# Kernel optimization log

Measured on AMD Instinct MI355X. Metric: run time of the kernel, lower is better.

Reference implementation:

```python
import jax, jax.numpy as jnp
import numpy as np

N_NODES = 50000
N_EDGES = 800000
DIM = 96
N_LAYERS = 3
N_GRAPHS = 128
OUT_DIM = 10


def setup_inputs() -> dict:
    key = jax.random.key(0)
    ks = jax.random.split(key, 9)
    s = 1.0 / np.sqrt(DIM)
    return {
        "x": jax.random.normal(ks[0], (N_NODES, DIM), dtype=jnp.float32),
        "edge_index": jax.random.randint(ks[1], (2, N_EDGES), 0, N_NODES, dtype=jnp.int32),
        "batch": jnp.sort(jax.random.randint(ks[2], (N_NODES,), 0, N_GRAPHS, dtype=jnp.int32)),
        "W1": jax.random.normal(ks[3], (N_LAYERS, DIM, DIM), dtype=jnp.float32) * s,
        "W2": jax.random.normal(ks[4], (N_LAYERS, DIM, DIM), dtype=jnp.float32) * s,
        "cw1": jax.random.normal(ks[5], (DIM, DIM), dtype=jnp.float32) * s,
        "cb1": jax.random.normal(ks[6], (DIM,), dtype=jnp.float32) * s,
        "cw2": jax.random.normal(ks[7], (DIM, OUT_DIM), dtype=jnp.float32) * s,
        "cb2": jax.random.normal(ks[8], (OUT_DIM,), dtype=jnp.float32) * s,
    }


def reference(x, edge_index, batch, W1, W2, cw1, cb1, cw2, cb2):
    src, dst = edge_index[0], edge_index[1]
    h = x
    for l in range(N_LAYERS):
        self_part = h @ W1[l]                       # [N, D]
        # transform at node level then gather per edge (same math as per-edge W2(x_j))
        msg = (h @ W2[l])[src]                      # [E, D]
        neighbor_part = jax.ops.segment_sum(msg, dst, num_segments=N_NODES)
        h = jax.nn.relu(self_part + neighbor_part)
    graph_emb = jax.ops.segment_sum(h, batch, num_segments=N_GRAPHS)  # [G, D]
    hidden = jax.nn.relu(graph_emb @ cw1 + cb1)
    return hidden @ cw2 + cb2                       # [G, OUT_DIM]
```

## Files before the change

### kernel.cpp

```cpp
#include <hip/hip_runtime.h>

#define N_NODES   50000
#define N_EDGES   800000
#define DIM       96
#define N_GRAPHS  128
#define OUT_DIM   10
#define NPAD      50048
#define NBINS     391
#define P1_BLOCKS 128
#define EPB       (N_EDGES / P1_BLOCKS)
#define SLICECAP  48
#define CAP       64
#define LPAD      104

#define CAST_NB   ((N_NODES * 12 + 255) / 256)
#define CONV_NB   ((3 * DIM * 2 * DIM + 255) / 256)

typedef __attribute__((ext_vector_type(8))) short          short8;
typedef __attribute__((ext_vector_type(8))) unsigned short u16x8;
typedef __attribute__((ext_vector_type(4))) float          f32x4;

__device__ __forceinline__ float b2f(unsigned short u) {
    union { unsigned int i; float f; } v; v.i = ((unsigned int)u) << 16; return v.f;
}
__device__ __forceinline__ unsigned short f2b(float f) {
    union { float f; unsigned int i; } v; v.f = f;
    unsigned int u = v.i;
    return (unsigned short)((u + 0x7fffu + ((u >> 16) & 1u)) >> 16);
}

__global__ __launch_bounds__(256) void prep(const float* __restrict__ x,
                                            const float* __restrict__ W1,
                                            const float* __restrict__ W2,
                                            unsigned short* __restrict__ harr,
                                            unsigned short* __restrict__ Bt)
{
    const int b = blockIdx.x;
    const int t = threadIdx.x;
    if (b < CAST_NB) {
        const int tid = b * 256 + t;
        if (tid >= N_NODES * 12) return;
        const int node = tid / 12;
        const int c    = (tid - node * 12) * 8;
        const float4 v0 = *(const float4*)(x + (size_t)node * DIM + c);
        const float4 v1 = *(const float4*)(x + (size_t)node * DIM + c + 4);
        u16x8 o;
        o[0] = f2b(v0.x); o[1] = f2b(v0.y); o[2] = f2b(v0.z); o[3] = f2b(v0.w);
        o[4] = f2b(v1.x); o[5] = f2b(v1.y); o[6] = f2b(v1.z); o[7] = f2b(v1.w);
        *(u16x8*)(harr + (size_t)node * DIM + c) = o;
    } else {
        const int idx = (b - CAST_NB) * 256 + t;
        if (idx >= 3 * DIM * 2 * DIM) return;
        const int l   = idx / (DIM * 2 * DIM);
        const int rem = idx - l * (DIM * 2 * DIM);
        const int n   = rem / (2 * DIM);
        const int k   = rem - n * (2 * DIM);
        const float v = (k < DIM) ? W1[(size_t)l * DIM * DIM + k * DIM + n]
                                  : W2[(size_t)l * DIM * DIM + (k - DIM) * DIM + n];
        Bt[idx] = f2b(v);
    }
}

__global__ __launch_bounds__(256) void pass1_bin(const int* __restrict__ src,
                                                 const int* __restrict__ dst,
                                                 int* __restrict__ binned,
                                                 int* __restrict__ cnt)
{
    __shared__ int cur[NBINS];
    const int t   = threadIdx.x;
    const int blk = blockIdx.x;
    const int e0  = blk * EPB;

    for (int b = t; b < NBINS; b += 256) cur[b] = 0;
    __syncthreads();

    for (int e = e0 + t; e < e0 + EPB; e += 256) {
        const int d   = dst[e];
        const int bin = d >> 7;
        const int pos = atomicAdd(&cur[bin], 1);
        if (pos < SLICECAP)
            binned[((size_t)bin * P1_BLOCKS + blk) * SLICECAP + pos]
                = ((d & 127) << 16) | src[e];
    }
    __syncthreads();

    for (int b = t; b < NBINS; b += 256)
        cnt[b * P1_BLOCKS + blk] = min(cur[b], SLICECAP);
}

__global__ __launch_bounds__(256) void pass2_scatter(const int* __restrict__ cnt,
                                                     const int* __restrict__ binned,
                                                     int* __restrict__ csrc,
                                                     int* __restrict__ deg)
{
    __shared__ int buf[2][P1_BLOCKS];
    __shared__ int soff[P1_BLOCKS + 1];
    __shared__ int ncnt[128];
    const int bin = blockIdx.x;
    const int t   = threadIdx.x;
    const int n0  = bin << 7;

    if (t < P1_BLOCKS) { buf[0][t] = cnt[bin * P1_BLOCKS + t]; ncnt[t] = 0; }
    __syncthreads();

    int c = 0;
#pragma unroll
    for (int off = 1; off < P1_BLOCKS; off <<= 1) {
        if (t < P1_BLOCKS) {
            int x = buf[c][t];
            if (t >= off) x += buf[c][t - off];
            buf[c ^ 1][t] = x;
        }
        __syncthreads();
        c ^= 1;
    }
    if (t < P1_BLOCKS) { soff[t + 1] = buf[c][t]; if (t == 0) soff[0] = 0; }
    __syncthreads();

    const int Eb = soff[P1_BLOCKS];
    for (int i = t; i < Eb; i += 256) {
        int lo = 0, hi = P1_BLOCKS - 1;
        while (lo < hi) { int mid = (lo + hi + 1) >> 1;
                          if (soff[mid] <= i) lo = mid; else hi = mid - 1; }
        const int v    = binned[((size_t)bin * P1_BLOCKS + lo) * SLICECAP + (i - soff[lo])];
        const int dlow = v >> 16;
        const int s    = v & 0xffff;
        const int pos  = atomicAdd(&ncnt[dlow], 1);
        if (pos < CAP) csrc[(size_t)(n0 + dlow) * CAP + pos] = s;
    }
    __syncthreads();

    if (t < 128 && n0 + t < N_NODES) deg[n0 + t] = min(ncnt[t], CAP);
}

__global__ __launch_bounds__(384) void gnn_layer(
    const unsigned short* __restrict__ harr, const int* __restrict__ deg,
    const int* __restrict__ csrc, const unsigned short* __restrict__ Btl,
    unsigned short* __restrict__ hout)
{
    __shared__ unsigned short aggLds[64][LPAD];
    const int t       = threadIdx.x;
    const int rowBase = blockIdx.x * 64;

    const int lane = t & 63;
    const int w    = t >> 6;
    const int m    = lane & 15;
    const int q    = lane >> 4;
    short8 bfrag[6];
#pragma unroll
    for (int s = 0; s < 6; s++)
        bfrag[s] = *(const short8*)(Btl + (size_t)(w * 16 + m) * (2 * DIM) + s * 32 + q * 8);

    {
        const int r    = t / 6;
        const int sub  = t - r * 6;
        const int node = rowBase + r;
        const int off  = sub * 16;

        float a[16];
#pragma unroll
        for (int i = 0; i < 16; i++) a[i] = 0.f;

        if (node < N_NODES) {
            const int d = deg[node];
            const int* __restrict__ bkt = csrc + (size_t)node * CAP;
            const unsigned short* __restrict__ hb = harr + off;

            const int nfull = d & ~3;
            int c = 0;
            for (; c < nfull; c += 4) {
                const int4 s = *(const int4*)(bkt + c);
                const unsigned short* p0 = hb + (size_t)s.x * DIM;
                const unsigned short* p1 = hb + (size_t)s.y * DIM;
                const unsigned short* p2 = hb + (size_t)s.z * DIM;
                const unsigned short* p3 = hb + (size_t)s.w * DIM;
                const u16x8 va0 = *(const u16x8*)(p0), vb0 = *(const u16x8*)(p0 + 8);
                const u16x8 va1 = *(const u16x8*)(p1), vb1 = *(const u16x8*)(p1 + 8);
                const u16x8 va2 = *(const u16x8*)(p2), vb2 = *(const u16x8*)(p2 + 8);
                const u16x8 va3 = *(const u16x8*)(p3), vb3 = *(const u16x8*)(p3 + 8);
#pragma unroll
                for (int i = 0; i < 8; i++) {
                    a[i]     += b2f(va0[i]) + b2f(va1[i]) + b2f(va2[i]) + b2f(va3[i]);
                    a[i + 8] += b2f(vb0[i]) + b2f(vb1[i]) + b2f(vb2[i]) + b2f(vb3[i]);
                }
            }
            for (; c < d; c++) {
                const unsigned short* p0 = hb + (size_t)bkt[c] * DIM;
                const u16x8 va0 = *(const u16x8*)(p0), vb0 = *(const u16x8*)(p0 + 8);
#pragma unroll
                for (int i = 0; i < 8; i++) {
                    a[i]     += b2f(va0[i]);
                    a[i + 8] += b2f(vb0[i]);
                }
            }
        }

        u16x8 o0, o1;
#pragma unroll
        for (int i = 0; i < 8; i++) { o0[i] = f2b(a[i]); o1[i] = f2b(a[i + 8]); }
        *(u16x8*)(&aggLds[r][off])     = o0;
        *(u16x8*)(&aggLds[r][off + 8]) = o1;
    }
    __syncthreads();

#pragma unroll
    for (int r = 0; r < 4; r++) {
        const int rb = rowBase + r * 16;
        f32x4 acc = {0.f, 0.f, 0.f, 0.f};
        const unsigned short* ah = harr + (size_t)(rb + m) * DIM + q * 8;
#pragma unroll
        for (int s = 0; s < 3; s++) {
            const short8 af = *(const short8*)(ah + s * 32);
            acc = __builtin_amdgcn_mfma_f32_16x16x32_bf16(af, bfrag[s], acc, 0, 0, 0);
        }
#pragma unroll
        for (int s = 0; s < 3; s++) {
            const short8 af = *(const short8*)(&aggLds[r * 16 + m][s * 32 + q * 8]);
            acc = __builtin_amdgcn_mfma_f32_16x16x32_bf16(af, bfrag[s + 3], acc, 0, 0, 0);
        }
#pragma unroll
        for (int i = 0; i < 4; i++) {
            const int grow = rb + q * 4 + i;
            if (grow < N_NODES)
                hout[(size_t)grow * DIM + w * 16 + m] = f2b(fmaxf(acc[i], 0.f));
        }
    }
}

__global__ __launch_bounds__(384) void pool_classify(
    const unsigned short* __restrict__ h, const int* __restrict__ batch,
    const float* __restrict__ cw1, const float* __restrict__ cb1,
    const float* __restrict__ cw2, const float* __restrict__ cb2,
    float* __restrict__ out)
{
    const int g = blockIdx.x;
    const int t = threadIdx.x;

    int lo = 0, hi = N_NODES;
    while (lo < hi) { int m = (lo + hi) >> 1; if (batch[m] < g) lo = m + 1; else hi = m; }
    const int start = lo;
    hi = N_NODES;
    while (lo < hi) { int m = (lo + hi) >> 1; if (batch[m] < g + 1) lo = m + 1; else hi = m; }
    const int end = lo;

    __shared__ float part[4][DIM];
    __shared__ float gr[DIM];
    __shared__ float hid[DIM];

    const int col = t % DIM;
    const int ty  = t / DIM;

    float s = 0.f;
    for (int n = start + ty; n < end; n += 4)
        s += b2f(h[(size_t)n * DIM + col]);
    part[ty][col] = s;
    __syncthreads();
    if (ty == 0)
        gr[col] = part[0][col] + part[1][col] + part[2][col] + part[3][col];
    __syncthreads();

    float hsum = 0.f;
    const int k0 = ty * (DIM / 4);
#pragma unroll 4
    for (int k = k0; k < k0 + DIM / 4; k++)
        hsum += gr[k] * cw1[k * DIM + col];
    part[ty][col] = hsum;
    __syncthreads();
    if (ty == 0)
        hid[col] = fmaxf(part[0][col] + part[1][col] + part[2][col] + part[3][col]
                         + cb1[col], 0.f);
    __syncthreads();

    if (t < OUT_DIM) {
        float o = cb2[t];
#pragma unroll 4
        for (int k = 0; k < DIM; k++) o += hid[k] * cw2[k * OUT_DIM + t];
        out[g * OUT_DIM + t] = o;
    }
}

extern "C" void kernel_launch(void* const* d_in, const int* in_sizes, int n_in,
                              void* d_out, int out_size, void* d_ws, size_t ws_size,
                              hipStream_t stream)
{
    const float* x     = (const float*)d_in[0];
    const int*   ei    = (const int*)  d_in[1];
    const int*   batch = (const int*)  d_in[2];
    const float* W1    = (const float*)d_in[3];
    const float* W2    = (const float*)d_in[4];
    const float* cw1   = (const float*)d_in[5];
    const float* cb1   = (const float*)d_in[6];
    const float* cw2   = (const float*)d_in[7];
    const float* cb2   = (const float*)d_in[8];
    float*       out   = (float*)d_out;

    const int* src = ei;
    const int* dst = ei + N_EDGES;

    unsigned short* bufA = (unsigned short*)d_ws;
    unsigned short* bufB = bufA + (size_t)NPAD * DIM;
    unsigned short* Bt   = bufB + (size_t)NPAD * DIM;
    int*   cnt    = (int*)(Bt + 3 * DIM * 2 * DIM);
    int*   binned = cnt + NBINS * P1_BLOCKS;
    int*   csrc   = binned + (size_t)NBINS * P1_BLOCKS * SLICECAP;
    int*   deg    = csrc + (size_t)N_NODES * CAP;

    prep<<<CAST_NB + CONV_NB, 256, 0, stream>>>(x, W1, W2, bufA, Bt);
    pass1_bin<<<P1_BLOCKS, 256, 0, stream>>>(src, dst, binned, cnt);
    pass2_scatter<<<NBINS, 256, 0, stream>>>(cnt, binned, csrc, deg);

    unsigned short* hin  = bufA;
    unsigned short* hout = bufB;
    for (int l = 0; l < 3; l++) {
        gnn_layer<<<NPAD / 64, 384, 0, stream>>>(hin, deg, csrc,
                                                 Bt + (size_t)l * DIM * 2 * DIM, hout);
        unsigned short* tmp = hin; hin = hout; hout = tmp;
    }

    pool_classify<<<N_GRAPHS, 384, 0, stream>>>(hin, batch, cw1, cb1, cw2, cb2, out);
}
```

Before: 275.9 us.

## Fuse prep with edge binning, simplify scatter, coalesce layer stores, widen pooling

The edge-binning pass is merged into the prep kernel so the x cast, weight transpose and binning share one launch. Pass2 drops its prefix scan and binary search and instead gives each slice to two threads that read it directly. The layer kernel stages its ReLU output in LDS and writes rows with 16-byte vector stores instead of scattered 2-byte stores. Pooling runs 960 threads per graph to spread the node reduction wider. The costs are an extra LDS round trip with two barriers per layer block, and pass2 load imbalance across slices.

```diff
diff --git a/kernel.cpp b/kernel.cpp
--- a/kernel.cpp
+++ b/kernel.cpp
@@ -29,16 +29,34 @@
     return (unsigned short)((u + 0x7fffu + ((u >> 16) & 1u)) >> 16);
 }
 
-__global__ __launch_bounds__(256) void prep(const float* __restrict__ x,
-                                            const float* __restrict__ W1,
-                                            const float* __restrict__ W2,
-                                            unsigned short* __restrict__ harr,
-                                            unsigned short* __restrict__ Bt)
-{
+__global__ __launch_bounds__(256) void prep_pass1(
+    const float* __restrict__ x,  const float* __restrict__ W1,
+    const float* __restrict__ W2, const int* __restrict__ src,
+    const int* __restrict__ dst,  unsigned short* __restrict__ harr,
+    unsigned short* __restrict__ Bt, int* __restrict__ binned,
+    int* __restrict__ cnt)
+{
+    __shared__ int cur[NBINS];
     const int b = blockIdx.x;
     const int t = threadIdx.x;
-    if (b < CAST_NB) {
-        const int tid = b * 256 + t;
+
+    if (b < P1_BLOCKS) {
+        const int e0 = b * EPB;
+        for (int i = t; i < NBINS; i += 256) cur[i] = 0;
+        __syncthreads();
+        for (int e = e0 + t; e < e0 + EPB; e += 256) {
+            const int d   = dst[e];
+            const int bin = d >> 7;
+            const int pos = atomicAdd(&cur[bin], 1);
+            if (pos < SLICECAP)
+                binned[((size_t)bin * P1_BLOCKS + b) * SLICECAP + pos]
+                    = ((d & 127) << 16) | src[e];
+        }
+        __syncthreads();
+        for (int i = t; i < NBINS; i += 256)
+            cnt[i * P1_BLOCKS + b] = min(cur[i], SLICECAP);
+    } else if (b < P1_BLOCKS + CAST_NB) {
+        const int tid = (b - P1_BLOCKS) * 256 + t;
         if (tid >= N_NODES * 12) return;
         const int node = tid / 12;
         const int c    = (tid - node * 12) * 8;
@@ -49,7 +67,7 @@
         o[4] = f2b(v1.x); o[5] = f2b(v1.y); o[6] = f2b(v1.z); o[7] = f2b(v1.w);
         *(u16x8*)(harr + (size_t)node * DIM + c) = o;
     } else {
-        const int idx = (b - CAST_NB) * 256 + t;
+        const int idx = (b - P1_BLOCKS - CAST_NB) * 256 + t;
         if (idx >= 3 * DIM * 2 * DIM) return;
         const int l   = idx / (DIM * 2 * DIM);
         const int rem = idx - l * (DIM * 2 * DIM);
@@ -61,68 +79,26 @@
     }
 }
 
-__global__ __launch_bounds__(256) void pass1_bin(const int* __restrict__ src,
-                                                 const int* __restrict__ dst,
-                                                 int* __restrict__ binned,
-                                                 int* __restrict__ cnt)
-{
-    __shared__ int cur[NBINS];
-    const int t   = threadIdx.x;
-    const int blk = blockIdx.x;
-    const int e0  = blk * EPB;
-
-    for (int b = t; b < NBINS; b += 256) cur[b] = 0;
-    __syncthreads();
-
-    for (int e = e0 + t; e < e0 + EPB; e += 256) {
-        const int d   = dst[e];
-        const int bin = d >> 7;
-        const int pos = atomicAdd(&cur[bin], 1);
-        if (pos < SLICECAP)
-            binned[((size_t)bin * P1_BLOCKS + blk) * SLICECAP + pos]
-                = ((d & 127) << 16) | src[e];
-    }
-    __syncthreads();
-
-    for (int b = t; b < NBINS; b += 256)
-        cnt[b * P1_BLOCKS + blk] = min(cur[b], SLICECAP);
-}
-
 __global__ __launch_bounds__(256) void pass2_scatter(const int* __restrict__ cnt,
                                                      const int* __restrict__ binned,
                                                      int* __restrict__ csrc,
                                                      int* __restrict__ deg)
 {
-    __shared__ int buf[2][P1_BLOCKS];
-    __shared__ int soff[P1_BLOCKS + 1];
     __shared__ int ncnt[128];
     const int bin = blockIdx.x;
     const int t   = threadIdx.x;
     const int n0  = bin << 7;
 
-    if (t < P1_BLOCKS) { buf[0][t] = cnt[bin * P1_BLOCKS + t]; ncnt[t] = 0; }
-    __syncthreads();
-
-    int c = 0;
-#pragma unroll
-    for (int off = 1; off < P1_BLOCKS; off <<= 1) {
-        if (t < P1_BLOCKS) {
-            int x = buf[c][t];
-            if (t >= off) x += buf[c][t - off];
-            buf[c ^ 1][t] = x;
-        }
-        __syncthreads();
-        c ^= 1;
-    }
-    if (t < P1_BLOCKS) { soff[t + 1] = buf[c][t]; if (t == 0) soff[0] = 0; }
-    __syncthreads();
-
-    const int Eb = soff[P1_BLOCKS];
-    for (int i = t; i < Eb; i += 256) {
-        int lo = 0, hi = P1_BLOCKS - 1;
-        while (lo < hi) { int mid = (lo + hi + 1) >> 1;
-                          if (soff[mid] <= i) lo = mid; else hi = mid - 1; }
-        const int v    = binned[((size_t)bin * P1_BLOCKS + lo) * SLICECAP + (i - soff[lo])];
+    if (t < 128) ncnt[t] = 0;
+    __syncthreads();
+
+    const int slice = t >> 1;
+    const int par   = t & 1;
+    const int c     = cnt[bin * P1_BLOCKS + slice];
+    const int* __restrict__ bb = binned + ((size_t)bin * P1_BLOCKS + slice) * SLICECAP;
+
+    for (int i = par; i < c; i += 2) {
+        const int v    = bb[i];
         const int dlow = v >> 16;
         const int s    = v & 0xffff;
         const int pos  = atomicAdd(&ncnt[dlow], 1);
@@ -203,6 +179,7 @@
     }
     __syncthreads();
 
+    f32x4 accv[4];
 #pragma unroll
     for (int r = 0; r < 4; r++) {
         const int rb = rowBase + r * 16;
@@ -218,16 +195,30 @@
             const short8 af = *(const short8*)(&aggLds[r * 16 + m][s * 32 + q * 8]);
             acc = __builtin_amdgcn_mfma_f32_16x16x32_bf16(af, bfrag[s + 3], acc, 0, 0, 0);
         }
-#pragma unroll
-        for (int i = 0; i < 4; i++) {
-            const int grow = rb + q * 4 + i;
-            if (grow < N_NODES)
-                hout[(size_t)grow * DIM + w * 16 + m] = f2b(fmaxf(acc[i], 0.f));
-        }
-    }
-}
-
-__global__ __launch_bounds__(384) void pool_classify(
+        accv[r] = acc;
+    }
+    __syncthreads();
+
+#pragma unroll
+    for (int r = 0; r < 4; r++)
+#pragma unroll
+        for (int i = 0; i < 4; i++)
+            aggLds[r * 16 + q * 4 + i][w * 16 + m] = f2b(fmaxf(accv[r][i], 0.f));
+    __syncthreads();
+
+#pragma unroll
+    for (int k = 0; k < 2; k++) {
+        const int idx = t + k * 384;
+        const int row = idx / 12;
+        const int ch  = idx - row * 12;
+        const int grow = rowBase + row;
+        if (grow < N_NODES)
+            *(u16x8*)(hout + (size_t)grow * DIM + ch * 8)
+                = *(const u16x8*)(&aggLds[row][ch * 8]);
+    }
+}
+
+__global__ __launch_bounds__(960) void pool_classify(
     const unsigned short* __restrict__ h, const int* __restrict__ batch,
     const float* __restrict__ cw1, const float* __restrict__ cb1,
     const float* __restrict__ cw2, const float* __restrict__ cb2,
@@ -243,7 +234,7 @@
     while (lo < hi) { int m = (lo + hi) >> 1; if (batch[m] < g + 1) lo = m + 1; else hi = m; }
     const int end = lo;
 
-    __shared__ float part[4][DIM];
+    __shared__ float part[10][DIM];
     __shared__ float gr[DIM];
     __shared__ float hid[DIM];
 
@@ -251,20 +242,26 @@
     const int ty  = t / DIM;
 
     float s = 0.f;
-    for (int n = start + ty; n < end; n += 4)
+    for (int n = start + ty; n < end; n += 10)
         s += b2f(h[(size_t)n * DIM + col]);
     part[ty][col] = s;
     __syncthreads();
-    if (ty == 0)
-        gr[col] = part[0][col] + part[1][col] + part[2][col] + part[3][col];
-    __syncthreads();
-
-    float hsum = 0.f;
-    const int k0 = ty * (DIM / 4);
+    if (ty == 0) {
+        float acc = 0.f;
+#pragma unroll
+        for (int p = 0; p < 10; p++) acc += part[p][col];
+        gr[col] = acc;
+    }
+    __syncthreads();
+
+    if (ty < 4) {
+        float hsum = 0.f;
+        const int k0 = ty * (DIM / 4);
 #pragma unroll 4
-    for (int k = k0; k < k0 + DIM / 4; k++)
-        hsum += gr[k] * cw1[k * DIM + col];
-    part[ty][col] = hsum;
+        for (int k = k0; k < k0 + DIM / 4; k++)
+            hsum += gr[k] * cw1[k * DIM + col];
+        part[ty][col] = hsum;
+    }
     __syncthreads();
     if (ty == 0)
         hid[col] = fmaxf(part[0][col] + part[1][col] + part[2][col] + part[3][col]
@@ -305,8 +302,8 @@
     int*   csrc   = binned + (size_t)NBINS * P1_BLOCKS * SLICECAP;
     int*   deg    = csrc + (size_t)N_NODES * CAP;
 
-    prep<<<CAST_NB + CONV_NB, 256, 0, stream>>>(x, W1, W2, bufA, Bt);
-    pass1_bin<<<P1_BLOCKS, 256, 0, stream>>>(src, dst, binned, cnt);
+    prep_pass1<<<P1_BLOCKS + CAST_NB + CONV_NB, 256, 0, stream>>>(
+        x, W1, W2, src, dst, bufA, Bt, binned, cnt);
     pass2_scatter<<<NBINS, 256, 0, stream>>>(cnt, binned, csrc, deg);
 
     unsigned short* hin  = bufA;
@@ -317,5 +314,5 @@
         unsigned short* tmp = hin; hin = hout; hout = tmp;
     }
 
-    pool_classify<<<N_GRAPHS, 384, 0, stream>>>(hin, batch, cw1, cb1, cw2, cb2, out);
-}
+    pool_classify<<<N_GRAPHS, 960, 0, stream>>>(hin, batch, cw1, cb1, cw2, cb2, out);
+}
```

New measurement: 253.9 us. 1.09x faster.
